# Optimization experiments

Hardware: AMD Instinct MI355X
Metric: run time of the kernel (lower is better)

## Reference

```python
import jax, jax.numpy as jnp
import numpy as np

B, T, D, H = 4, 2048, 512, 8
DK = D // H

def setup_inputs() -> dict:
    key = jax.random.key(0)
    ks = jax.random.split(key, 5)
    s = 1.0 / np.sqrt(D)
    return {
        "x": jax.random.normal(ks[0], (B, T, D), dtype=jnp.float32),
        "Wq": jax.random.normal(ks[1], (D, D), dtype=jnp.float32) * s,
        "bq": jnp.zeros((D,), dtype=jnp.float32),
        "Wk": jax.random.normal(ks[2], (D, D), dtype=jnp.float32) * s,
        "bk": jnp.zeros((D,), dtype=jnp.float32),
        "Wv": jax.random.normal(ks[3], (D, D), dtype=jnp.float32) * s,
        "bv": jnp.zeros((D,), dtype=jnp.float32),
        "Wo": jax.random.normal(ks[4], (D, D), dtype=jnp.float32) * s,
        "bo": jnp.zeros((D,), dtype=jnp.float32),
    }

def reference(x, Wq, bq, Wk, bk, Wv, bv, Wo, bo):
    # Linear projections (torch Linear: x @ W.T + b); split into heads.
    q = (x @ Wq.T + bq).reshape(B, T, H, DK)  # [B,T,H,dk]
    k = (x @ Wk.T + bk).reshape(B, T, H, DK)
    v = (x @ Wv.T + bv).reshape(B, T, H, DK)
    scale = 1.0 / np.sqrt(DK)
    # scores: [B,H,T,T]
    scores = jnp.einsum("bqhd,bkhd->bhqk", q, k) * scale
    attn = jax.nn.softmax(scores, axis=-1)
    ctx = jnp.einsum("bhqk,bkhd->bqhd", attn, v).reshape(B, T, D)
    return ctx @ Wo.T + bo
```

## Files before the change

kernel.cpp:

```cpp
#include <hip/hip_runtime.h>
#include <stdint.h>

#define NB 4
#define NT 2048
#define ND 512
#define NH 8
#define NDK 64
#define NM (NB*NT)

typedef __attribute__((ext_vector_type(8))) short short8;
typedef __attribute__((ext_vector_type(4))) float f32x4;

__device__ __forceinline__ unsigned short f2b(float f) {
    union { float f; uint32_t u; } v; v.f = f;
    return (unsigned short)((v.u + 0x7FFFu + ((v.u >> 16) & 1u)) >> 16);
}

__device__ __forceinline__ void load_lds16(const void* g, void* l) {
    void* gn = const_cast<void*>(g);
    __builtin_amdgcn_global_load_lds((__attribute__((address_space(1))) void*)gn,
                                     (__attribute__((address_space(3))) void*)l,
                                     16, 0, 0);
}

__global__ void convert_all(const float* __restrict__ x,  const float* __restrict__ wq,
                            const float* __restrict__ wk, const float* __restrict__ wv,
                            const float* __restrict__ wo, unsigned short* __restrict__ dst) {
    size_t i = ((size_t)blockIdx.x * 256 + threadIdx.x) * 4;
    const float* src; size_t off;
    if (i < 4194304) { src = x; off = i; }
    else {
        size_t j = i - 4194304;
        src = (j < 262144) ? wq : (j < 524288) ? wk : (j < 786432) ? wv : wo;
        off = j & 262143;
    }
    f32x4 v = *(const f32x4*)(src + off);
    ushort4 r;
    r.x = f2b(v[0]); r.y = f2b(v[1]); r.z = f2b(v[2]); r.w = f2b(v[3]);
    *(ushort4*)(dst + i) = r;
}

__global__ __launch_bounds__(256, 3) void proj_gemm(
        const unsigned short* __restrict__ X,
        const unsigned short* __restrict__ Wbase,
        const float* __restrict__ bias0, const float* __restrict__ bias1,
        const float* __restrict__ bias2,
        unsigned short* __restrict__ Obase, unsigned short* __restrict__ VTb,
        float scale0) {
    const int z = blockIdx.z;
    const float* bias = (z == 0) ? bias0 : (z == 1 ? bias1 : bias2);
    const float scale = (z == 0) ? scale0 : 1.0f;

    int rowBase, colBase;
    const unsigned short *Ap, *Bp;
    if (z == 2) {
        rowBase = blockIdx.x * 128;  colBase = blockIdx.y * 128;
        Ap = Wbase + 2 * (ND * ND);  Bp = X;
    } else {
        rowBase = blockIdx.y * 128;  colBase = blockIdx.x * 128;
        Ap = X;                      Bp = Wbase + (size_t)z * (ND * ND);
    }

    __shared__ alignas(16) unsigned short ldsA[128 * 64];
    __shared__ alignas(16) unsigned short ldsW[128 * 64];

    const int tid = threadIdx.x;
    const int lane = tid & 63, wave = tid >> 6;
    const int quad = lane >> 4, l15 = lane & 15;
    const int wm = wave >> 1, wn = wave & 1;

    const int rS = tid >> 3;
    const int gc = (tid & 7) ^ (rS & 7);
    const unsigned short* gA = Ap + (size_t)(rowBase + rS) * ND + gc * 8;
    const unsigned short* gW = Bp + (size_t)(colBase + rS) * ND + gc * 8;
    const int ldst = wave * 512;

    const int swz = l15 & 7;

    f32x4 acc[4][4];
#pragma unroll
    for (int i = 0; i < 4; i++)
#pragma unroll
        for (int j = 0; j < 4; j++) acc[i][j] = (f32x4)0.0f;

    for (int kt = 0; kt < ND / 64; ++kt) {
        __syncthreads();
#pragma unroll
        for (int c = 0; c < 4; ++c) {
            load_lds16(gA + (size_t)c * 32 * ND, ldsA + c * 2048 + ldst);
            load_lds16(gW + (size_t)c * 32 * ND, ldsW + c * 2048 + ldst);
        }
        gA += 64; gW += 64;
        __syncthreads();

        __builtin_amdgcn_s_setprio(1);
#pragma unroll
        for (int ks = 0; ks < 2; ++ks) {
            short8 af[4], bfm[4];
#pragma unroll
            for (int mt = 0; mt < 4; ++mt)
                af[mt] = *(const short8*)(ldsA + (wm * 64 + mt * 16 + l15) * 64
                                          + (((ks * 4 + quad) ^ swz) * 8));
#pragma unroll
            for (int nt = 0; nt < 4; ++nt)
                bfm[nt] = *(const short8*)(ldsW + (wn * 64 + nt * 16 + l15) * 64
                                           + (((ks * 4 + quad) ^ swz) * 8));
#pragma unroll
            for (int mt = 0; mt < 4; ++mt)
#pragma unroll
                for (int nt = 0; nt < 4; ++nt)
                    acc[mt][nt] = __builtin_amdgcn_mfma_f32_16x16x32_bf16(
                        af[mt], bfm[nt], acc[mt][nt], 0, 0, 0);
        }
        __builtin_amdgcn_s_setprio(0);
    }

    if (z == 2) {
        const int bz = colBase >> 11;
        const int t0 = colBase & 2047;
        unsigned short* VTo = VTb + ((size_t)(bz * 512 + rowBase)) * NT + t0;
#pragma unroll
        for (int mt = 0; mt < 4; mt++)
#pragma unroll
            for (int reg = 0; reg < 4; reg++) {
                int m = wm * 64 + mt * 16 + quad * 4 + reg;
                float bm = bias[rowBase + m];
                unsigned short* dst = VTo + (size_t)m * NT + wn * 64 + l15;
#pragma unroll
                for (int nt = 0; nt < 4; nt++)
                    dst[nt * 16] = f2b(acc[mt][nt][reg] + bm);
            }
    } else {
        float biasr[4];
#pragma unroll
        for (int nt = 0; nt < 4; nt++)
            biasr[nt] = bias[colBase + wn * 64 + nt * 16 + l15];
        unsigned short* Oz = Obase + (size_t)z * ((size_t)NM * ND);
#pragma unroll
        for (int mt = 0; mt < 4; mt++) {
            int row = rowBase + wm * 64 + mt * 16 + quad * 4;
#pragma unroll
            for (int reg = 0; reg < 4; reg++) {
                unsigned short* dst = Oz + (size_t)(row + reg) * ND + colBase + wn * 64 + l15;
#pragma unroll
                for (int nt = 0; nt < 4; nt++)
                    dst[nt * 16] = f2b((acc[mt][nt][reg] + biasr[nt]) * scale);
            }
        }
    }
}

__global__ __launch_bounds__(256, 4) void out_gemm(
        const unsigned short* __restrict__ A, const unsigned short* __restrict__ W,
        const float* __restrict__ bias, float* __restrict__ OF) {
    __shared__ alignas(16) unsigned short ldsA[64 * 64];
    __shared__ alignas(16) unsigned short ldsW[128 * 64];

    const int tid = threadIdx.x;
    const int lane = tid & 63, wave = tid >> 6;
    const int quad = lane >> 4, l15 = lane & 15;
    const int wm = wave >> 1, wn = wave & 1;
    const int rowBase = blockIdx.y * 64;
    const int colBase = blockIdx.x * 128;

    const int rS = tid >> 3;
    const int gc = (tid & 7) ^ (rS & 7);
    const unsigned short* gA = A + (size_t)(rowBase + rS) * ND + gc * 8;
    const unsigned short* gW = W + (size_t)(colBase + rS) * ND + gc * 8;
    const int ldst = wave * 512;
    const int swz = l15 & 7;

    f32x4 acc[2][4];
#pragma unroll
    for (int mt = 0; mt < 2; mt++)
#pragma unroll
        for (int nt = 0; nt < 4; nt++) acc[mt][nt] = (f32x4)0.0f;

    for (int kt = 0; kt < ND / 64; ++kt) {
        __syncthreads();
#pragma unroll
        for (int c = 0; c < 2; ++c)
            load_lds16(gA + (size_t)c * 32 * ND, ldsA + c * 2048 + ldst);
#pragma unroll
        for (int c = 0; c < 4; ++c)
            load_lds16(gW + (size_t)c * 32 * ND, ldsW + c * 2048 + ldst);
        gA += 64; gW += 64;
        __syncthreads();

        __builtin_amdgcn_s_setprio(1);
#pragma unroll
        for (int ks = 0; ks < 2; ++ks) {
            short8 af[2], bfm[4];
#pragma unroll
            for (int mt = 0; mt < 2; ++mt)
                af[mt] = *(const short8*)(ldsA + (wm * 32 + mt * 16 + l15) * 64
                                          + (((ks * 4 + quad) ^ swz) * 8));
#pragma unroll
            for (int nt = 0; nt < 4; ++nt)
                bfm[nt] = *(const short8*)(ldsW + (wn * 64 + nt * 16 + l15) * 64
                                           + (((ks * 4 + quad) ^ swz) * 8));
#pragma unroll
            for (int mt = 0; mt < 2; ++mt)
#pragma unroll
                for (int nt = 0; nt < 4; ++nt)
                    acc[mt][nt] = __builtin_amdgcn_mfma_f32_16x16x32_bf16(
                        af[mt], bfm[nt], acc[mt][nt], 0, 0, 0);
        }
        __builtin_amdgcn_s_setprio(0);
    }

    float biasr[4];
#pragma unroll
    for (int nt = 0; nt < 4; nt++)
        biasr[nt] = bias[colBase + wn * 64 + nt * 16 + l15];

#pragma unroll
    for (int mt = 0; mt < 2; mt++)
#pragma unroll
        for (int reg = 0; reg < 4; reg++) {
            int row = rowBase + wm * 32 + mt * 16 + quad * 4 + reg;
            float* dst = OF + (size_t)row * ND + colBase + wn * 64 + l15;
#pragma unroll
            for (int nt = 0; nt < 4; nt++)
                dst[nt * 16] = acc[mt][nt][reg] + biasr[nt];
        }
}

__global__ __launch_bounds__(512, 4) void attn_kernel(
        const unsigned short* __restrict__ Qb, const unsigned short* __restrict__ Kb,
        const unsigned short* __restrict__ VTb, unsigned short* __restrict__ Cb) {
    const int L = blockIdx.x + 16 * (blockIdx.y + 8 * blockIdx.z);
    const int s = L >> 3;
    const int qt = s & 15;
    const int g = (L & 7) + 8 * (s >> 4);
    const int h = g & 7, b = g >> 3;

    __shared__ alignas(16) unsigned short Ks[2 * 8192];
    __shared__ alignas(16) unsigned short Vt[2 * 8192];

    const int tid = threadIdx.x, lane = tid & 63, wave = tid >> 6;
    const int wq = wave & 3, half = wave >> 2;
    const int quad = lane >> 4, l15 = lane & 15;
    const size_t headOff = (size_t)h * NDK;
    const size_t rowB = (size_t)b * NT;
    const unsigned short* VT = VTb + (size_t)(b * NH + h) * ((size_t)NDK * NT);

    short8 aq[2][2];
#pragma unroll
    for (int t = 0; t < 2; ++t)
#pragma unroll
        for (int ks = 0; ks < 2; ++ks)
            aq[t][ks] = *(const short8*)(Qb
                + (rowB + qt * 128 + wq * 32 + t * 16 + l15) * ND
                + headOff + ks * 32 + quad * 8);

    const int rK = tid >> 3;
    const int rb = rK & 31;
    const int kap = (rb < 16) ? ((rb >> 2) * 8 + (rb & 3))
                              : (((rb - 16) >> 2) * 8 + 4 + ((rb - 16) & 3));
    const int gK8 = (tid & 7) ^ (rK & 7);
    const unsigned short* gK = Kb + (rowB + (rK & 32) + kap) * ND + headOff + gK8 * 8;
    const int rV = tid >> 4;
    const int gV8 = (tid & 15) ^ (rV & 7);
    const unsigned short* gV = VT + (size_t)rV * NT + gV8 * 8;
    const int ldst = wave * 512;

    const int swz = l15 & 7;
    const int ko0 = l15 * 64 + ((quad ^ swz) * 8);
    const int ko1 = l15 * 64 + (((4 + quad) ^ swz) * 8);

    const short8 ones = {0x3F80, 0x3F80, 0x3F80, 0x3F80,
                         0x3F80, 0x3F80, 0x3F80, 0x3F80};

    f32x4 o[2][4];
#pragma unroll
    for (int t = 0; t < 2; ++t)
#pragma unroll
        for (int nt = 0; nt < 4; ++nt) o[t][nt] = (f32x4)0.0f;
    f32x4 lsum[2] = {(f32x4)0.0f, (f32x4)0.0f};

    auto STAGE = [&](int bb, int r) {
        const unsigned short* k = gK + (size_t)r * 128 * ND;
        const unsigned short* v = gV + (size_t)r * 128;
        unsigned short* kd = Ks + bb * 8192 + ldst;
        unsigned short* vd = Vt + bb * 8192 + ldst;
#pragma unroll
        for (int c = 0; c < 2; ++c) {
            load_lds16(k + (size_t)c * 64 * ND, kd + c * 4096);
            load_lds16(v + (size_t)c * 32 * NT, vd + c * 4096);
        }
    };

    STAGE(0, 0);
    __syncthreads();

    for (int kv = 0; kv < 16; ++kv) {
        const int buf = kv & 1;
        if (kv < 15) STAGE(buf ^ 1, kv + 1);

        const unsigned short* KB = Ks + buf * 8192;
        const unsigned short* VB = Vt + buf * 8192;
        __builtin_amdgcn_s_setprio(1);
#pragma unroll
        for (int pp = 0; pp < 2; ++pp) {
            const int pb = half * 2 + pp;
            short8 kA0 = *(const short8*)(KB + pb * 2048 + ko0);
            short8 kA1 = *(const short8*)(KB + pb * 2048 + ko1);
            short8 kB0 = *(const short8*)(KB + pb * 2048 + 1024 + ko0);
            short8 kB1 = *(const short8*)(KB + pb * 2048 + 1024 + ko1);
            const int vo = l15 * 128 + (((pb * 4 + quad) ^ swz) * 8);
            short8 vf[4];
#pragma unroll
            for (int nt = 0; nt < 4; ++nt)
                vf[nt] = *(const short8*)(VB + vo + nt * 2048);

#pragma unroll
            for (int t = 0; t < 2; ++t) {
                f32x4 sa = (f32x4)0.0f, sb = (f32x4)0.0f;
                sa = __builtin_amdgcn_mfma_f32_16x16x32_bf16(kA0, aq[t][0], sa, 0, 0, 0);
                sa = __builtin_amdgcn_mfma_f32_16x16x32_bf16(kA1, aq[t][1], sa, 0, 0, 0);
                sb = __builtin_amdgcn_mfma_f32_16x16x32_bf16(kB0, aq[t][0], sb, 0, 0, 0);
                sb = __builtin_amdgcn_mfma_f32_16x16x32_bf16(kB1, aq[t][1], sb, 0, 0, 0);
                float pA0 = __builtin_amdgcn_exp2f(sa[0]), pA1 = __builtin_amdgcn_exp2f(sa[1]);
                float pA2 = __builtin_amdgcn_exp2f(sa[2]), pA3 = __builtin_amdgcn_exp2f(sa[3]);
                float pB0 = __builtin_amdgcn_exp2f(sb[0]), pB1 = __builtin_amdgcn_exp2f(sb[1]);
                float pB2 = __builtin_amdgcn_exp2f(sb[2]), pB3 = __builtin_amdgcn_exp2f(sb[3]);
                union { uint32_t w[4]; short8 v; } cv;
                cv.w[0] = __builtin_amdgcn_perm(__float_as_uint(pA1), __float_as_uint(pA0), 0x07060302u);
                cv.w[1] = __builtin_amdgcn_perm(__float_as_uint(pA3), __float_as_uint(pA2), 0x07060302u);
                cv.w[2] = __builtin_amdgcn_perm(__float_as_uint(pB1), __float_as_uint(pB0), 0x07060302u);
                cv.w[3] = __builtin_amdgcn_perm(__float_as_uint(pB3), __float_as_uint(pB2), 0x07060302u);
                lsum[t] = __builtin_amdgcn_mfma_f32_16x16x32_bf16(
                    cv.v, ones, lsum[t], 0, 0, 0);
#pragma unroll
                for (int nt = 0; nt < 4; ++nt)
                    o[t][nt] = __builtin_amdgcn_mfma_f32_16x16x32_bf16(
                        cv.v, vf[nt], o[t][nt], 0, 0, 0);
            }
        }
        __builtin_amdgcn_s_setprio(0);
        __syncthreads();
    }

    f32x4* sc4  = (f32x4*)Ks;
    f32x4* scl4 = (f32x4*)Vt;
    const int lx = lane & 7;
    const int base = wq * 64 + lane;
    if (half) {
#pragma unroll
        for (int t = 0; t < 2; ++t) {
            scl4[base * 2 + (t ^ (lane & 1))] = lsum[t];
#pragma unroll
            for (int nt = 0; nt < 4; ++nt)
                sc4[base * 8 + ((t * 4 + nt) ^ lx)] = o[t][nt];
        }
    }
    __syncthreads();
    if (!half) {
#pragma unroll
        for (int t = 0; t < 2; ++t) {
            lsum[t] += scl4[base * 2 + (t ^ (lane & 1))];
#pragma unroll
            for (int nt = 0; nt < 4; ++nt)
                o[t][nt] += sc4[base * 8 + ((t * 4 + nt) ^ lx)];
#pragma unroll
            for (int reg = 0; reg < 4; ++reg) {
                float inv = 1.0f / lsum[t][reg];
                size_t row = rowB + qt * 128 + wq * 32 + t * 16 + quad * 4 + reg;
#pragma unroll
                for (int nt = 0; nt < 4; ++nt)
                    Cb[row * ND + headOff + nt * 16 + l15] = f2b(o[t][nt][reg] * inv);
            }
        }
    }
}

extern "C" void kernel_launch(void* const* d_in, const int* in_sizes, int n_in,
                              void* d_out, int out_size, void* d_ws, size_t ws_size,
                              hipStream_t stream) {
    (void)in_sizes; (void)n_in; (void)out_size; (void)ws_size;
    const float* x  = (const float*)d_in[0];
    const float* Wq = (const float*)d_in[1];
    const float* bq = (const float*)d_in[2];
    const float* Wk = (const float*)d_in[3];
    const float* bk = (const float*)d_in[4];
    const float* Wv = (const float*)d_in[5];
    const float* bv = (const float*)d_in[6];
    const float* Wo = (const float*)d_in[7];
    const float* bo = (const float*)d_in[8];
    float* out = (float*)d_out;

    unsigned short* ws  = (unsigned short*)d_ws;
    unsigned short* xb  = ws;
    unsigned short* wqb = xb + 4194304;
    unsigned short* Qb  = wqb + 4 * 262144;
    unsigned short* Kb  = Qb + 4194304;
    unsigned short* VTb = Kb + 4194304;
    unsigned short* Cb  = VTb + 4194304;
    unsigned short* wob = wqb + 3 * 262144;

    convert_all<<<5120, 256, 0, stream>>>(x, Wq, Wk, Wv, Wo, ws);

    const float qscale = 0.125f * 1.44269504f;
    proj_gemm<<<dim3(4, 64, 3), 256, 0, stream>>>(xb, wqb, bq, bk, bv, Qb, VTb, qscale);
    attn_kernel<<<dim3(16, 8, 4), 512, 0, stream>>>(Qb, Kb, VTb, Cb);
    out_gemm<<<dim3(4, 128), 256, 0, stream>>>(Cb, wob, bo, out);
}
```

Measured before the change: 150.5 us.

## Load V fragments directly from global into registers, drop V LDS staging

The attention kernel no longer stages V^T tiles through shared memory. Each wave now reads its V fragments straight from global memory into registers at the start of every KV step, and the LDS footprint shrinks to the K double buffer plus a small reduction scratch area. This also drops the s_setprio calls around the MFMA loops in both projection GEMMs. The aim is to cut LDS traffic and LDS allocation, which may raise occupancy, but the direct global loads are exposed latency that is no longer prefetched a stage ahead, and V rows are now read redundantly by the four query waves in each half.

```diff
diff --git a/kernel.cpp b/kernel.cpp
--- a/kernel.cpp
+++ b/kernel.cpp
@@ -93,7 +93,6 @@
         gA += 64; gW += 64;
         __syncthreads();
 
-        __builtin_amdgcn_s_setprio(1);
 #pragma unroll
         for (int ks = 0; ks < 2; ++ks) {
             short8 af[4], bfm[4];
@@ -112,7 +111,6 @@
                     acc[mt][nt] = __builtin_amdgcn_mfma_f32_16x16x32_bf16(
                         af[mt], bfm[nt], acc[mt][nt], 0, 0, 0);
         }
-        __builtin_amdgcn_s_setprio(0);
     }
 
     if (z == 2) {
@@ -187,7 +185,6 @@
         gA += 64; gW += 64;
         __syncthreads();
 
-        __builtin_amdgcn_s_setprio(1);
 #pragma unroll
         for (int ks = 0; ks < 2; ++ks) {
             short8 af[2], bfm[4];
@@ -206,7 +203,6 @@
                     acc[mt][nt] = __builtin_amdgcn_mfma_f32_16x16x32_bf16(
                         af[mt], bfm[nt], acc[mt][nt], 0, 0, 0);
         }
-        __builtin_amdgcn_s_setprio(0);
     }
 
     float biasr[4];
@@ -235,8 +231,7 @@
     const int g = (L & 7) + 8 * (s >> 4);
     const int h = g & 7, b = g >> 3;
 
-    __shared__ alignas(16) unsigned short Ks[2 * 8192];
-    __shared__ alignas(16) unsigned short Vt[2 * 8192];
+    __shared__ alignas(16) unsigned short Ks[2 * 8192 + 4096];
 
     const int tid = threadIdx.x, lane = tid & 63, wave = tid >> 6;
     const int wq = wave & 3, half = wave >> 2;
@@ -260,10 +255,9 @@
                               : (((rb - 16) >> 2) * 8 + 4 + ((rb - 16) & 3));
     const int gK8 = (tid & 7) ^ (rK & 7);
     const unsigned short* gK = Kb + (rowB + (rK & 32) + kap) * ND + headOff + gK8 * 8;
-    const int rV = tid >> 4;
-    const int gV8 = (tid & 15) ^ (rV & 7);
-    const unsigned short* gV = VT + (size_t)rV * NT + gV8 * 8;
     const int ldst = wave * 512;
+
+    const unsigned short* gVd = VT + (size_t)l15 * NT + quad * 8;
 
     const int swz = l15 & 7;
     const int ko0 = l15 * 64 + ((quad ^ swz) * 8);
@@ -281,14 +275,10 @@
 
     auto STAGE = [&](int bb, int r) {
         const unsigned short* k = gK + (size_t)r * 128 * ND;
-        const unsigned short* v = gV + (size_t)r * 128;
         unsigned short* kd = Ks + bb * 8192 + ldst;
-        unsigned short* vd = Vt + bb * 8192 + ldst;
-#pragma unroll
-        for (int c = 0; c < 2; ++c) {
+#pragma unroll
+        for (int c = 0; c < 2; ++c)
             load_lds16(k + (size_t)c * 64 * ND, kd + c * 4096);
-            load_lds16(v + (size_t)c * 32 * NT, vd + c * 4096);
-        }
     };
 
     STAGE(0, 0);
@@ -296,10 +286,19 @@
 
     for (int kv = 0; kv < 16; ++kv) {
         const int buf = kv & 1;
+
+        short8 vfr[2][4];
+#pragma unroll
+        for (int pp = 0; pp < 2; ++pp)
+#pragma unroll
+            for (int nt = 0; nt < 4; ++nt)
+                vfr[pp][nt] = *(const short8*)(gVd + (size_t)nt * 16 * NT
+                                               + (half * 2 + pp) * 32);
+        gVd += 128;
+
         if (kv < 15) STAGE(buf ^ 1, kv + 1);
 
         const unsigned short* KB = Ks + buf * 8192;
-        const unsigned short* VB = Vt + buf * 8192;
         __builtin_amdgcn_s_setprio(1);
 #pragma unroll
         for (int pp = 0; pp < 2; ++pp) {
@@ -308,11 +307,6 @@
             short8 kA1 = *(const short8*)(KB + pb * 2048 + ko1);
             short8 kB0 = *(const short8*)(KB + pb * 2048 + 1024 + ko0);
             short8 kB1 = *(const short8*)(KB + pb * 2048 + 1024 + ko1);
-            const int vo = l15 * 128 + (((pb * 4 + quad) ^ swz) * 8);
-            short8 vf[4];
-#pragma unroll
-            for (int nt = 0; nt < 4; ++nt)
-                vf[nt] = *(const short8*)(VB + vo + nt * 2048);
 
 #pragma unroll
             for (int t = 0; t < 2; ++t) {
@@ -335,7 +329,7 @@
 #pragma unroll
                 for (int nt = 0; nt < 4; ++nt)
                     o[t][nt] = __builtin_amdgcn_mfma_f32_16x16x32_bf16(
-                        cv.v, vf[nt], o[t][nt], 0, 0, 0);
+                        cv.v, vfr[pp][nt], o[t][nt], 0, 0, 0);
             }
         }
         __builtin_amdgcn_s_setprio(0);
@@ -343,7 +337,7 @@
     }
 
     f32x4* sc4  = (f32x4*)Ks;
-    f32x4* scl4 = (f32x4*)Vt;
+    f32x4* scl4 = (f32x4*)(Ks + 16384);
     const int lx = lane & 7;
     const int base = wq * 64 + lane;
     if (half) {
```

Result: slower. 186.7 us (+24.1%).
